# Performance work log

Measured on AMD Instinct MI355X. Metric: run time of the kernel, lower is better.

Reference implementation:

```python
import jax, jax.numpy as jnp
import numpy as np

D_MODEL = 1024
N_HEADS = 16
HEAD_DIM = D_MODEL // N_HEADS


def setup_inputs() -> dict:
    key = jax.random.key(0)
    ks = jax.random.split(key, 5)
    B, S = 4, 2048
    scale = 1.0 / np.sqrt(D_MODEL)
    return {
        "x": jax.random.normal(ks[0], (B, S, D_MODEL), dtype=jnp.float32),
        "wq": jax.random.normal(ks[1], (D_MODEL, D_MODEL), dtype=jnp.float32) * scale,
        "wk": jax.random.normal(ks[2], (D_MODEL, D_MODEL), dtype=jnp.float32) * scale,
        "wv": jax.random.normal(ks[3], (D_MODEL, D_MODEL), dtype=jnp.float32) * scale,
        "wo": jax.random.normal(ks[4], (D_MODEL, D_MODEL), dtype=jnp.float32) * scale,
    }


def reference(x, wq, wk, wv, wo):
    B, S, _ = x.shape
    # projections: x @ W.T, then split heads -> [B, H, S, hd]
    def split_heads(t):
        return t.reshape(B, S, N_HEADS, HEAD_DIM).transpose(0, 2, 1, 3)

    q = split_heads(x @ wq.T)
    k = split_heads(x @ wk.T)
    v = split_heads(x @ wv.T)

    # scores [B, H, S, S], causal mask, stable softmax
    score = jnp.einsum("bhqd,bhkd->bhqk", q, k) / np.sqrt(HEAD_DIM)
    causal = jnp.tril(jnp.ones((S, S), dtype=bool))
    score = jnp.where(causal, score, -jnp.inf)
    attn = jax.nn.softmax(score, axis=-1)

    out = jnp.einsum("bhqk,bhkd->bhqd", attn, v)
    out = out.transpose(0, 2, 1, 3).reshape(B, S, D_MODEL)
    return out @ wo.T
```

## Files before the change

kernel.cpp:

```cpp
#include <hip/hip_runtime.h>
#include <type_traits>


typedef unsigned short u16;
typedef __attribute__((ext_vector_type(8))) short s8;
typedef __attribute__((ext_vector_type(4))) float f4;

#if __has_builtin(__builtin_amdgcn_exp2f)
#define EXP2(x) __builtin_amdgcn_exp2f(x)
#else
#define EXP2(x) exp2f(x)
#endif

__device__ __forceinline__ u16 f2bf(float f) {
    union { float f; unsigned u; } v; v.f = f;
    unsigned r = v.u + 0x7fffu + ((v.u >> 16) & 1u);
    return (u16)(r >> 16);
}

__device__ __forceinline__ unsigned pack_bf2(float a, float b) {
    return __builtin_amdgcn_perm(__float_as_uint(b), __float_as_uint(a),
                                 0x07060302u);
}

__device__ __forceinline__ void cp16(const void* g, void* l) {
    __builtin_amdgcn_global_load_lds(
        (const __attribute__((address_space(1))) unsigned int*)g,
        (__attribute__((address_space(3))) unsigned int*)l, 16, 0, 0);
}

__device__ __forceinline__ s8 load8f(const float* p) {
    const float4 lo = *(const float4*)p;
    const float4 hi = *(const float4*)(p + 4);
    s8 r;
    r[0] = (short)f2bf(lo.x); r[1] = (short)f2bf(lo.y);
    r[2] = (short)f2bf(lo.z); r[3] = (short)f2bf(lo.w);
    r[4] = (short)f2bf(hi.x); r[5] = (short)f2bf(hi.y);
    r[6] = (short)f2bf(hi.z); r[7] = (short)f2bf(hi.w);
    return r;
}

__global__ __launch_bounds__(256)
void f32_to_bf16(const float* __restrict__ in, u16* __restrict__ out, int n8)
{
    const int i = blockIdx.x * 256 + threadIdx.x;
    if (i < n8) *(s8*)(out + (size_t)i * 8) = load8f(in + (size_t)i * 8);
}

__global__ __launch_bounds__(256)
void cvt_w3(const float* __restrict__ a, const float* __restrict__ b2,
            const float* __restrict__ c3, u16* __restrict__ o, int per)
{
    const int y = blockIdx.y;
    const float* src = (y == 0) ? a : ((y == 1) ? b2 : c3);
    u16* dst = o + (size_t)y * per;
    const int i = blockIdx.x * 256 + threadIdx.x;
    *(s8*)(dst + (size_t)i * 8) = load8f(src + (size_t)i * 8);
}

template<typename TC>
__global__ __launch_bounds__(256)
void gemm_bb(const u16* __restrict__ A,
             const u16* __restrict__ W0, const u16* __restrict__ W1,
             const u16* __restrict__ W2,
             TC* __restrict__ C0, TC* __restrict__ C1,
             u16* __restrict__ VT, int K, float cscale)
{
    __shared__ u16 As[2][128 * 32];
    __shared__ u16 Bs[2][128 * 32];

    const int t  = threadIdx.x;
    const int bm = blockIdx.x;
    const int nglob = blockIdx.y * 128;

    const u16* W; int nloc, mode;
    if (nglob < 1024)      { W = W0; nloc = nglob;        mode = 0; }
    else if (nglob < 2048) { W = W1; nloc = nglob - 1024; mode = 1; }
    else                   { W = W2; nloc = nglob - 2048; mode = 2; }

    const int lane = t & 63, w = t >> 6;
    const int wm = (w >> 1) * 64, wn = (w & 1) * 64;
    const int quad = lane >> 4, l16 = lane & 15;

    const int sc = (((lane & 3) ^ ((lane >> 3) & 3))) * 8;
    const int sr = w * 32 + (lane >> 2);
    const u16* Ag0 = A + (size_t)(bm * 128 + sr) * K + sc;
    const u16* Ag1 = Ag0 + (size_t)16 * K;
    const u16* Wg0 = W + (size_t)(nloc + sr) * K + sc;
    const u16* Wg1 = Wg0 + (size_t)16 * K;
    const int la0 = (w * 32) * 32;
    const int la1 = (w * 32 + 16) * 32;

    const int ca = (quad ^ ((l16 >> 1) & 3)) * 8;

    auto stage = [&](int buf, int k0) {
        cp16(Ag0 + k0, &As[buf][la0]);
        cp16(Ag1 + k0, &As[buf][la1]);
        cp16(Wg0 + k0, &Bs[buf][la0]);
        cp16(Wg1 + k0, &Bs[buf][la1]);
    };

    f4 acc[4][4];
    for (int i = 0; i < 4; i++)
        for (int j = 0; j < 4; j++)
            acc[i][j] = (f4){0.f, 0.f, 0.f, 0.f};

    stage(0, 0);
    int cur = 0;
    for (int k0 = 0; k0 < K; k0 += 32) {
        __syncthreads();
        if (k0 + 32 < K) stage(cur ^ 1, k0 + 32);

        s8 af[4], bf[4];
        for (int i = 0; i < 4; i++)
            af[i] = *(const s8*)&As[cur][(wm + i * 16 + l16) * 32 + ca];
        for (int j = 0; j < 4; j++)
            bf[j] = *(const s8*)&Bs[cur][(wn + j * 16 + l16) * 32 + ca];
        for (int i = 0; i < 4; i++)
            for (int j = 0; j < 4; j++)
                acc[i][j] = __builtin_amdgcn_mfma_f32_16x16x32_bf16(
                                af[i], bf[j], acc[i][j], 0, 0, 0);
        cur ^= 1;
    }

    if (mode == 2) {
        for (int i = 0; i < 4; i++) {
            const int row0 = bm * 128 + wm + i * 16 + quad * 4;
            const int b = row0 >> 11, s = row0 & 2047;
            for (int j = 0; j < 4; j++) {
                const int n = nloc + wn + j * 16 + l16;
                const int h = n >> 6, d = n & 63;
                unsigned lo = ((unsigned)f2bf(acc[i][j][1]) << 16) | f2bf(acc[i][j][0]);
                unsigned hi = ((unsigned)f2bf(acc[i][j][3]) << 16) | f2bf(acc[i][j][2]);
                *(uint2*)(VT + ((size_t)((b * 16 + h) * 64 + d)) * 2048 + s) =
                    make_uint2(lo, hi);
            }
        }
    } else {
        TC* C = (mode == 0) ? C0 : C1;
        const float cs = (mode == 0) ? cscale : 1.0f;
        for (int i = 0; i < 4; i++) {
            const int row = bm * 128 + wm + i * 16 + quad * 4;
            for (int j = 0; j < 4; j++) {
                const int col = nloc + wn + j * 16 + l16;
                for (int r = 0; r < 4; r++) {
                    const float val = acc[i][j][r] * cs;
                    if constexpr (std::is_same<TC, float>::value)
                        C[(size_t)(row + r) * 1024 + col] = val;
                    else
                        C[(size_t)(row + r) * 1024 + col] = f2bf(val);
                }
            }
        }
    }
}

#define PSTR 72

__global__ __launch_bounds__(256)
void attn_q32(const u16* __restrict__ Q, const u16* __restrict__ K,
              const u16* __restrict__ Vt, u16* __restrict__ O)
{
    __shared__ u16 Ks[2][64 * 64];
    __shared__ u16 Vs[2][64 * 64];
    __shared__ u16 Ps[4][32 * PSTR];

    const int bh = blockIdx.x;
    const int p  = 15 - blockIdx.y;
    const int h  = bh & 15, b = bh >> 4;

    const int t = threadIdx.x, lane = t & 63, w = t >> 6;
    const int quad = lane >> 4, l16 = lane & 15;
    const int colH = h * 64;

    const int q32 = 4 * p + w;
    const int ktw = q32 / 2 + 1;
    const int ktb = 2 * p + 2;

    s8 ones;
    for (int e = 0; e < 8; e++) ones[e] = (short)0x3F80;

    const int vrow = lane >> 3;
    const int scc  = ((lane & 7) ^ vrow) * 8;
    const int r0   = w * 16 + vrow;
    const u16* Kg0 = K  + ((size_t)b * 2048 + r0) * 1024 + colH + scc;
    const u16* Kg1 = Kg0 + (size_t)8 * 1024;
    const u16* Vg0 = Vt + ((size_t)(b * 16 + h) * 64 + r0) * 2048 + scc;
    const u16* Vg1 = Vg0 + (size_t)8 * 2048;
    const int kl0 = (w * 16) * 64;
    const int kl1 = (w * 16 + 8) * 64;

    auto stageKV = [&](int buf, int kt) {
        cp16(Kg0 + (size_t)kt * 65536, &Ks[buf][kl0]);
        cp16(Kg1 + (size_t)kt * 65536, &Ks[buf][kl1]);
        cp16(Vg0 + kt * 64, &Vs[buf][kl0]);
        cp16(Vg1 + kt * 64, &Vs[buf][kl1]);
    };

    const size_t rowQ0 = (size_t)b * 2048 + q32 * 32;

    s8 qf[2][2];
    for (int i = 0; i < 2; i++)
        for (int kk = 0; kk < 2; kk++)
            qf[i][kk] = *(const s8*)&Q[(rowQ0 + i * 16 + l16) * 1024 +
                                       colH + kk * 32 + quad * 8];

    f4 o_acc[2][4];
    f4 l_acc[2];
    for (int i = 0; i < 2; i++) {
        l_acc[i] = (f4){0.f, 0.f, 0.f, 0.f};
        for (int j = 0; j < 4; j++)
            o_acc[i][j] = (f4){0.f, 0.f, 0.f, 0.f};
    }

    stageKV(0, 0);
    int cur = 0;

    for (int kt = 0; kt < ktb; ++kt) {
        __syncthreads();
        if (kt + 1 < ktb) stageKV(cur ^ 1, kt + 1);

        if (kt < ktw) {
            f4 sa[4][2];
            for (int j = 0; j < 4; j++)
                for (int i = 0; i < 2; i++)
                    sa[j][i] = (f4){0.f, 0.f, 0.f, 0.f};
            for (int kk = 0; kk < 2; kk++) {
                s8 kf[4];
                for (int j = 0; j < 4; j++)
                    kf[j] = *(const s8*)&Ks[cur][(j * 16 + l16) * 64 +
                                            (((kk * 4 + quad) ^ (l16 & 7)) * 8)];
                for (int j = 0; j < 4; j++)
                    for (int i = 0; i < 2; i++)
                        sa[j][i] = __builtin_amdgcn_mfma_f32_16x16x32_bf16(
                                       kf[j], qf[i][kk], sa[j][i], 0, 0, 0);
            }

            const bool diag = (kt == ktw - 1);
            for (int i = 0; i < 2; i++) {
                const int q_l = i * 16 + l16;
                const int q_g = q32 * 32 + q_l;
                for (int j = 0; j < 4; j++) {
                    const int kv0 = kt * 64 + j * 16 + quad * 4;
                    float p0 = EXP2(sa[j][i][0]);
                    float p1 = EXP2(sa[j][i][1]);
                    float p2 = EXP2(sa[j][i][2]);
                    float p3 = EXP2(sa[j][i][3]);
                    if (diag) {
                        if (kv0 + 0 > q_g) p0 = 0.f;
                        if (kv0 + 1 > q_g) p1 = 0.f;
                        if (kv0 + 2 > q_g) p2 = 0.f;
                        if (kv0 + 3 > q_g) p3 = 0.f;
                    }
                    *(uint2*)&Ps[w][q_l * PSTR + j * 16 + quad * 4] =
                        make_uint2(pack_bf2(p0, p1), pack_bf2(p2, p3));
                }
            }

            for (int kk = 0; kk < 2; kk++) {
                s8 pf[2], vf[4];
                for (int i = 0; i < 2; i++)
                    pf[i] = *(const s8*)&Ps[w][(i * 16 + l16) * PSTR +
                                               kk * 32 + quad * 8];
                for (int jd = 0; jd < 4; jd++)
                    vf[jd] = *(const s8*)&Vs[cur][(jd * 16 + l16) * 64 +
                                            (((kk * 4 + quad) ^ (l16 & 7)) * 8)];
                for (int i = 0; i < 2; i++)
                    l_acc[i] = __builtin_amdgcn_mfma_f32_16x16x32_bf16(
                                   pf[i], ones, l_acc[i], 0, 0, 0);
                for (int i = 0; i < 2; i++)
                    for (int jd = 0; jd < 4; jd++)
                        o_acc[i][jd] = __builtin_amdgcn_mfma_f32_16x16x32_bf16(
                                           pf[i], vf[jd], o_acc[i][jd], 0, 0, 0);
            }
        }
        cur ^= 1;
    }

    for (int i = 0; i < 2; i++) {
        float rinv[4];
        for (int r = 0; r < 4; r++) rinv[r] = 1.0f / l_acc[i][r];
        for (int jd = 0; jd < 4; jd++)
            for (int r = 0; r < 4; r++) {
                const size_t row = rowQ0 + i * 16 + quad * 4 + r;
                O[row * 1024 + colH + jd * 16 + l16] =
                    f2bf(o_acc[i][jd][r] * rinv[r]);
            }
    }
}

extern "C" void kernel_launch(void* const* d_in, const int* in_sizes, int n_in,
                              void* d_out, int out_size, void* d_ws, size_t ws_size,
                              hipStream_t stream)
{
    const float* x  = (const float*)d_in[0];
    const float* wq = (const float*)d_in[1];
    const float* wk = (const float*)d_in[2];
    const float* wv = (const float*)d_in[3];
    const float* wo = (const float*)d_in[4];
    float* out = (float*)d_out;

    const size_t MD = (size_t)8192 * 1024;
    const size_t WD = (size_t)1024 * 1024;
    u16* Qb  = (u16*)d_ws;
    u16* Kb  = Qb + MD;
    u16* Vtb = Kb + MD;
    u16* Xb  = Vtb + MD;
    u16* Wqkv = (u16*)d_out;
    u16* Ob  = Qb;
    u16* Wob = Kb;

    f32_to_bf16<<<4096, 256, 0, stream>>>(x, Xb, (int)(MD / 8));

    cvt_w3<<<dim3(512, 3), 256, 0, stream>>>(wq, wk, wv, Wqkv, (int)WD);

    gemm_bb<u16><<<dim3(64, 24), 256, 0, stream>>>(
        Xb, Wqkv, Wqkv + WD, Wqkv + 2 * WD, Qb, Kb, Vtb, 1024, 0.18033688f);

    attn_q32<<<dim3(64, 16), 256, 0, stream>>>(Qb, Kb, Vtb, Ob);

    f32_to_bf16<<<512, 256, 0, stream>>>(wo, Wob, (int)(WD / 8));

    gemm_bb<float><<<dim3(64, 8), 256, 0, stream>>>(
        Ob, Wob, Wob, Wob, out, out, nullptr, 1024, 1.0f);
}
```

Baseline: 243.0 us.

## Widen projection GEMM tiles to 128x256 with 8 waves and interleaved prefetch

The projection GEMM kernel now uses 512-thread blocks computing 128x256 output tiles with a K-step of 64. It uses an XOR-swizzled LDS layout, splits the next-tile async copies between MFMA groups, and raises wave priority with s_setprio around the MFMA bursts. The intent is more reuse of each A tile, fewer barriers per K, and better overlap of global loads with matrix math. In exchange LDS use rises to 96 KB per block and the grid shrinks, so the output GEMM launches only 256 blocks, which may underfill the GPU.

```diff
diff --git a/kernel.cpp b/kernel.cpp
--- a/kernel.cpp
+++ b/kernel.cpp
@@ -59,19 +59,19 @@
 }
 
 template<typename TC>
-__global__ __launch_bounds__(256)
-void gemm_bb(const u16* __restrict__ A,
-             const u16* __restrict__ W0, const u16* __restrict__ W1,
-             const u16* __restrict__ W2,
-             TC* __restrict__ C0, TC* __restrict__ C1,
-             u16* __restrict__ VT, int K, float cscale)
-{
-    __shared__ u16 As[2][128 * 32];
-    __shared__ u16 Bs[2][128 * 32];
+__global__ __launch_bounds__(512)
+void gemm8(const u16* __restrict__ A,
+           const u16* __restrict__ W0, const u16* __restrict__ W1,
+           const u16* __restrict__ W2,
+           TC* __restrict__ C0, TC* __restrict__ C1,
+           u16* __restrict__ VT, int K, float cscale)
+{
+    __shared__ u16 As[2][128 * 64];
+    __shared__ u16 Bs[2][256 * 64];
 
     const int t  = threadIdx.x;
     const int bm = blockIdx.x;
-    const int nglob = blockIdx.y * 128;
+    const int nglob = blockIdx.y * 256;
 
     const u16* W; int nloc, mode;
     if (nglob < 1024)      { W = W0; nloc = nglob;        mode = 0; }
@@ -79,56 +79,126 @@
     else                   { W = W2; nloc = nglob - 2048; mode = 2; }
 
     const int lane = t & 63, w = t >> 6;
-    const int wm = (w >> 1) * 64, wn = (w & 1) * 64;
+    const int wr = w >> 2, wc = w & 3;
     const int quad = lane >> 4, l16 = lane & 15;
 
-    const int sc = (((lane & 3) ^ ((lane >> 3) & 3))) * 8;
-    const int sr = w * 32 + (lane >> 2);
-    const u16* Ag0 = A + (size_t)(bm * 128 + sr) * K + sc;
-    const u16* Ag1 = Ag0 + (size_t)16 * K;
-    const u16* Wg0 = W + (size_t)(nloc + sr) * K + sc;
-    const u16* Wg1 = Wg0 + (size_t)16 * K;
-    const int la0 = (w * 32) * 32;
-    const int la1 = (w * 32 + 16) * 32;
-
-    const int ca = (quad ^ ((l16 >> 1) & 3)) * 8;
-
-    auto stage = [&](int buf, int k0) {
-        cp16(Ag0 + k0, &As[buf][la0]);
-        cp16(Ag1 + k0, &As[buf][la1]);
-        cp16(Wg0 + k0, &Bs[buf][la0]);
-        cp16(Wg1 + k0, &Bs[buf][la1]);
-    };
+    const int r8 = lane >> 3;
+    const int scol = ((lane & 7) ^ r8) * 8;
+    const u16* Ag = A + (size_t)(bm * 128 + 16 * w + r8) * K + scol;
+    const u16* Wg = W + (size_t)(nloc + 32 * w + r8) * K + scol;
+    const int ldsA = (16 * w) * 64;
+    const int ldsB = (32 * w) * 64;
+
+    #define ARD(i, kk) (*(const s8*)&As[cur][(wr * 64 + (i) * 16 + l16) * 64 + \
+                        ((((kk) * 4 + quad) ^ (l16 & 7)) * 8)])
+    #define BRD(j, kk) (*(const s8*)&Bs[cur][(wc * 64 + (j) * 16 + l16) * 64 + \
+                        ((((kk) * 4 + quad) ^ (l16 & 7)) * 8)])
 
     f4 acc[4][4];
+    #pragma unroll
     for (int i = 0; i < 4; i++)
+        #pragma unroll
         for (int j = 0; j < 4; j++)
             acc[i][j] = (f4){0.f, 0.f, 0.f, 0.f};
 
-    stage(0, 0);
+    cp16(Ag, &As[0][ldsA]);
+    cp16(Ag + (size_t)8 * K, &As[0][ldsA + 8 * 64]);
+    #pragma unroll
+    for (int c = 0; c < 4; c++)
+        cp16(Wg + (size_t)(8 * c) * K, &Bs[0][ldsB + c * 8 * 64]);
+
+    const int NK = K >> 6;
     int cur = 0;
-    for (int k0 = 0; k0 < K; k0 += 32) {
-        __syncthreads();
-        if (k0 + 32 < K) stage(cur ^ 1, k0 + 32);
-
-        s8 af[4], bf[4];
-        for (int i = 0; i < 4; i++)
-            af[i] = *(const s8*)&As[cur][(wm + i * 16 + l16) * 32 + ca];
-        for (int j = 0; j < 4; j++)
-            bf[j] = *(const s8*)&Bs[cur][(wn + j * 16 + l16) * 32 + ca];
-        for (int i = 0; i < 4; i++)
-            for (int j = 0; j < 4; j++)
-                acc[i][j] = __builtin_amdgcn_mfma_f32_16x16x32_bf16(
-                                af[i], bf[j], acc[i][j], 0, 0, 0);
+    for (int kt = 0; kt < NK; ++kt) {
+        asm volatile("s_waitcnt vmcnt(0)\n\ts_barrier" ::: "memory");
+        const int nk0 = (kt + 1) << 6;
+        const bool more = (kt + 1 < NK);
+
+        s8 af[4][2], bfr[4][2];
+        #pragma unroll
+        for (int i = 0; i < 2; i++)
+            #pragma unroll
+            for (int kk = 0; kk < 2; kk++)
+                af[i][kk] = ARD(i, kk);
+        #pragma unroll
+        for (int j = 0; j < 2; j++)
+            #pragma unroll
+            for (int kk = 0; kk < 2; kk++)
+                bfr[j][kk] = BRD(j, kk);
+        if (more) {
+            cp16(Ag + nk0, &As[cur ^ 1][ldsA]);
+            cp16(Ag + nk0 + (size_t)8 * K, &As[cur ^ 1][ldsA + 8 * 64]);
+            cp16(Wg + nk0, &Bs[cur ^ 1][ldsB]);
+        }
+        __builtin_amdgcn_s_setprio(1);
+        #pragma unroll
+        for (int i = 0; i < 2; i++)
+            #pragma unroll
+            for (int j = 0; j < 2; j++)
+                #pragma unroll
+                for (int kk = 0; kk < 2; kk++)
+                    acc[i][j] = __builtin_amdgcn_mfma_f32_16x16x32_bf16(
+                                    af[i][kk], bfr[j][kk], acc[i][j], 0, 0, 0);
+        __builtin_amdgcn_s_setprio(0);
+        #pragma unroll
+        for (int j = 2; j < 4; j++)
+            #pragma unroll
+            for (int kk = 0; kk < 2; kk++)
+                bfr[j][kk] = BRD(j, kk);
+        if (more) {
+            #pragma unroll
+            for (int c = 1; c < 4; c++)
+                cp16(Wg + nk0 + (size_t)(8 * c) * K,
+                     &Bs[cur ^ 1][ldsB + c * 8 * 64]);
+        }
+        __builtin_amdgcn_s_setprio(1);
+        #pragma unroll
+        for (int i = 0; i < 2; i++)
+            #pragma unroll
+            for (int j = 2; j < 4; j++)
+                #pragma unroll
+                for (int kk = 0; kk < 2; kk++)
+                    acc[i][j] = __builtin_amdgcn_mfma_f32_16x16x32_bf16(
+                                    af[i][kk], bfr[j][kk], acc[i][j], 0, 0, 0);
+        __builtin_amdgcn_s_setprio(0);
+        #pragma unroll
+        for (int i = 2; i < 4; i++)
+            #pragma unroll
+            for (int kk = 0; kk < 2; kk++)
+                af[i][kk] = ARD(i, kk);
+        __builtin_amdgcn_s_setprio(1);
+        #pragma unroll
+        for (int i = 2; i < 4; i++)
+            #pragma unroll
+            for (int j = 0; j < 2; j++)
+                #pragma unroll
+                for (int kk = 0; kk < 2; kk++)
+                    acc[i][j] = __builtin_amdgcn_mfma_f32_16x16x32_bf16(
+                                    af[i][kk], bfr[j][kk], acc[i][j], 0, 0, 0);
+        __builtin_amdgcn_s_setprio(0);
+        __builtin_amdgcn_s_setprio(1);
+        #pragma unroll
+        for (int i = 2; i < 4; i++)
+            #pragma unroll
+            for (int j = 2; j < 4; j++)
+                #pragma unroll
+                for (int kk = 0; kk < 2; kk++)
+                    acc[i][j] = __builtin_amdgcn_mfma_f32_16x16x32_bf16(
+                                    af[i][kk], bfr[j][kk], acc[i][j], 0, 0, 0);
+        __builtin_amdgcn_s_setprio(0);
         cur ^= 1;
     }
+    #undef ARD
+    #undef BRD
 
     if (mode == 2) {
+        #pragma unroll
         for (int i = 0; i < 4; i++) {
-            const int row0 = bm * 128 + wm + i * 16 + quad * 4;
+            const int row0 = bm * 128 + wr * 64 + i * 16 + quad * 4;
             const int b = row0 >> 11, s = row0 & 2047;
+            #pragma unroll
             for (int j = 0; j < 4; j++) {
-                const int n = nloc + wn + j * 16 + l16;
+                const int n = nloc + wc * 64 + j * 16 + l16;
                 const int h = n >> 6, d = n & 63;
                 unsigned lo = ((unsigned)f2bf(acc[i][j][1]) << 16) | f2bf(acc[i][j][0]);
                 unsigned hi = ((unsigned)f2bf(acc[i][j][3]) << 16) | f2bf(acc[i][j][2]);
@@ -139,10 +209,13 @@
     } else {
         TC* C = (mode == 0) ? C0 : C1;
         const float cs = (mode == 0) ? cscale : 1.0f;
+        #pragma unroll
         for (int i = 0; i < 4; i++) {
-            const int row = bm * 128 + wm + i * 16 + quad * 4;
+            const int row = bm * 128 + wr * 64 + i * 16 + quad * 4;
+            #pragma unroll
             for (int j = 0; j < 4; j++) {
-                const int col = nloc + wn + j * 16 + l16;
+                const int col = nloc + wc * 64 + j * 16 + l16;
+                #pragma unroll
                 for (int r = 0; r < 4; r++) {
                     const float val = acc[i][j][r] * cs;
                     if constexpr (std::is_same<TC, float>::value)
@@ -314,13 +387,13 @@
 
     cvt_w3<<<dim3(512, 3), 256, 0, stream>>>(wq, wk, wv, Wqkv, (int)WD);
 
-    gemm_bb<u16><<<dim3(64, 24), 256, 0, stream>>>(
+    gemm8<u16><<<dim3(64, 12), 512, 0, stream>>>(
         Xb, Wqkv, Wqkv + WD, Wqkv + 2 * WD, Qb, Kb, Vtb, 1024, 0.18033688f);
 
     attn_q32<<<dim3(64, 16), 256, 0, stream>>>(Qb, Kb, Vtb, Ob);
 
     f32_to_bf16<<<512, 256, 0, stream>>>(wo, Wob, (int)(WD / 8));
 
-    gemm_bb<float><<<dim3(64, 8), 256, 0, stream>>>(
+    gemm8<float><<<dim3(64, 4), 512, 0, stream>>>(
         Ob, Wob, Wob, Wob, out, out, nullptr, 1024, 1.0f);
 }
```

Result: slower. 250.7 us (+3.2%).
